# Kernel optimization log

Hardware: AMD Instinct MI355X
Metric: run time of the kernel (lower is better)

Reference implementation:

```python
import jax, jax.numpy as jnp
import numpy as np

N = 100000      # nodes
E = 1600000     # edges
IN, H, OUT = 128, 128, 64
P_DROP = 0.5


def _glorot_linear(key, out_d, in_d):
    # PyG Linear default init (kaiming-uniform-ish); exact init is irrelevant for the baseline
    bound = 1.0 / np.sqrt(in_d)
    return jax.random.uniform(key, (out_d, in_d), jnp.float32, -bound, bound)


def setup_inputs() -> dict:
    key = jax.random.key(0)
    ks = jax.random.split(key, 8)
    x = jax.random.normal(ks[0], (N, IN), jnp.float32)
    edge_index = jax.random.randint(ks[1], (2, E), 0, N, dtype=jnp.int64)
    W1l = _glorot_linear(ks[2], H, IN)
    b1 = jnp.zeros((H,), jnp.float32)
    W1r = _glorot_linear(ks[3], H, IN)
    W2l = _glorot_linear(ks[4], OUT, H)
    b2 = jnp.zeros((OUT,), jnp.float32)
    W2r = _glorot_linear(ks[5], OUT, H)
    return dict(x=x, edge_index=edge_index, W1l=W1l, b1=b1, W1r=W1r,
                W2l=W2l, b2=b2, W2r=W2r)


def _sage_conv(x, src, dst, Wl, bl, Wr):
    # PyG SAGEConv (aggr='mean'): out = lin_l(mean_{j in N(i)} x_j) + lin_r(x_i)
    msg = x[src]                                             # [E, d] gather
    agg = jax.ops.segment_sum(msg, dst, num_segments=N)      # [N, d] scatter-add
    cnt = jax.ops.segment_sum(jnp.ones((src.shape[0], 1), x.dtype), dst,
                              num_segments=N)                # [N, 1] in-degree
    mean = agg / jnp.maximum(cnt, 1.0)                       # isolated nodes -> 0
    return mean @ Wl.T + bl + x @ Wr.T


def reference(x, edge_index, W1l, b1, W1r, W2l, b2, W2r):
    src, dst = edge_index[0], edge_index[1]
    h = _sage_conv(x, src, dst, W1l, b1, W1r)
    h = jax.nn.relu(h)
    # F.dropout(p=0.5) made deterministic with a fixed key
    keep = jax.random.bernoulli(jax.random.key(42), 1.0 - P_DROP, h.shape)
    h = jnp.where(keep, h / (1.0 - P_DROP), 0.0)
    return _sage_conv(h, src, dst, W2l, b2, W2r)
```

## Files before the change

### kernel.cpp

```cpp
#include <hip/hip_runtime.h>
#include <hip/hip_bf16.h>

#define N_NODES 100000
#define NE      1600000

#define BINSH 7
#define NBIN  782
#define BCAP  3072
#define SEPB  16384
#define NBLK  ((NE + SEPB - 1) / SEPB)
#define NMASKW 200000

typedef __attribute__((ext_vector_type(8))) short bfrag;
typedef __attribute__((ext_vector_type(4))) float ffrag;

#define BFLO(u) __uint_as_float((u) << 16)
#define BFHI(u) __uint_as_float((u) & 0xffff0000u)

__device__ __forceinline__ unsigned tf_rotl(unsigned x, int d) {
    return (x << d) | (x >> (32 - d));
}

__device__ __forceinline__ unsigned tf_word(unsigned f) {
    const unsigned ks0 = 0u;
    const unsigned ks1 = 42u;
    const unsigned ks2 = 0x1BD11BDAu ^ 0u ^ 42u;
    unsigned x0 = 0u + ks0;
    unsigned x1 = f + ks1;
#define TF_RND(r) { x0 += x1; x1 = tf_rotl(x1, r); x1 ^= x0; }
    TF_RND(13) TF_RND(15) TF_RND(26) TF_RND(6)
    x0 += ks1; x1 += ks2 + 1u;
    TF_RND(17) TF_RND(29) TF_RND(16) TF_RND(24)
    x0 += ks2; x1 += ks0 + 2u;
    TF_RND(13) TF_RND(15) TF_RND(26) TF_RND(6)
    x0 += ks0; x1 += ks1 + 3u;
    TF_RND(17) TF_RND(29) TF_RND(16) TF_RND(24)
    x0 += ks1; x1 += ks2 + 4u;
    TF_RND(13) TF_RND(15) TF_RND(26) TF_RND(6)
    x0 += ks2; x1 += ks0 + 5u;
#undef TF_RND
    return x0 ^ x1;
}

__device__ __forceinline__ unsigned short bf_bits(float v) {
    __hip_bfloat16 b = __float2bfloat16(v);
    return *(unsigned short*)&b;
}

__global__ __launch_bounds__(256) void k_pre(
    const float4* __restrict__ x4, ushort4* __restrict__ xb4,
    const float* __restrict__ W1l, const float* __restrict__ W1r,
    const float* __restrict__ W2l, const float* __restrict__ W2r,
    __hip_bfloat16* __restrict__ wb,
    const int* __restrict__ ei, int* __restrict__ flag,
    int* __restrict__ bincur, unsigned long long* __restrict__ km) {
    const int tid0 = blockIdx.x * 256 + threadIdx.x;
    const int stride = gridDim.x * 256;

    for (int i = tid0; i < N_NODES * 128 / 4; i += stride) {
        float4 v = x4[i];
        ushort4 o;
        o.x = bf_bits(v.x); o.y = bf_bits(v.y);
        o.z = bf_bits(v.z); o.w = bf_bits(v.w);
        xb4[i] = o;
    }
    for (int i = tid0; i < 49152; i += stride) {
        float v;
        if (i < 16384)      v = W1l[i];
        else if (i < 32768) v = W1r[i - 16384];
        else if (i < 40960) v = W2l[i - 32768];
        else                v = W2r[i - 40960];
        wb[i] = __float2bfloat16(v);
    }
    if (blockIdx.x == 0) {
        __shared__ int nz;
        if (threadIdx.x == 0) nz = 0;
        __syncthreads();
        for (int i = threadIdx.x; i < 1024; i += 256) {
            if (ei[2 * i + 1] != 0) atomicAdd(&nz, 1);
            bincur[i] = 0;
        }
        __syncthreads();
        if (threadIdx.x == 0) *flag = (nz == 0) ? 1 : 0;
    }
    const int lane = threadIdx.x & 63;
    const int gw = tid0 >> 6;
    const int nw = stride >> 6;
    for (int widx = gw; widx < NMASKW; widx += nw) {
        unsigned wv = tf_word((unsigned)widx * 64u + (unsigned)lane);
        unsigned long long keep = __ballot(!(wv & 0x80000000u));
        if (lane == 0) km[widx] = keep;
    }
}

__global__ __launch_bounds__(1024) void k_binscatter(const int* __restrict__ ei,
        const int* __restrict__ flag, int* __restrict__ bincur,
        int* __restrict__ pairs) {
    __shared__ int h[NBIN];
    __shared__ int lbase[NBIN];
    for (int i = threadIdx.x; i < NBIN; i += 1024) h[i] = 0;
    __syncthreads();
    const int is64 = *flag;
    const int e0 = blockIdx.x * SEPB + threadIdx.x;
    int d[16], s[16];
#pragma unroll
    for (int k = 0; k < 16; ++k) {
        int e = e0 + k * 1024;
        if (e < NE) {
            d[k] = is64 ? ei[2 * (NE + e)] : ei[NE + e];
            s[k] = is64 ? ei[2 * e]        : ei[e];
            atomicAdd(&h[d[k] >> BINSH], 1);
        } else {
            d[k] = -1; s[k] = 0;
        }
    }
    __syncthreads();
    for (int i = threadIdx.x; i < NBIN; i += 1024) {
        int c = h[i];
        lbase[i] = c ? atomicAdd(&bincur[i], c) : 0;
        h[i] = 0;
    }
    __syncthreads();
#pragma unroll
    for (int k = 0; k < 16; ++k) {
        if (d[k] >= 0) {
            int b = d[k] >> BINSH;
            int r = atomicAdd(&h[b], 1);
            pairs[(size_t)b * BCAP + lbase[b] + r] =
                ((d[k] & 127) << 17) | s[k];
        }
    }
}

__global__ __launch_bounds__(1024) void k_aggcsr(
        const __hip_bfloat16* __restrict__ feat,
        const int* __restrict__ pairs, const int* __restrict__ bincnt,
        int* __restrict__ ptr, int* __restrict__ adj,
        __hip_bfloat16* __restrict__ mean) {
    __shared__ int ladj[BCAP];
    __shared__ int cnt[128];
    __shared__ int sc[128];
    __shared__ int woff[128];
    __shared__ int red[16];
    __shared__ int base_s;
    const int b = blockIdx.x;
    const int t = threadIdx.x;

    int s = 0;
    for (int i = t; i < b; i += 1024) s += bincnt[i];
#pragma unroll
    for (int off = 32; off > 0; off >>= 1) s += __shfl_down(s, off);
    if ((t & 63) == 0) red[t >> 6] = s;
    if (t < 128) cnt[t] = 0;
    __syncthreads();
    if (t == 0) {
        int tot = 0;
#pragma unroll
        for (int i = 0; i < 16; ++i) tot += red[i];
        base_s = tot;
    }
    __syncthreads();
    const int base = base_s;
    const int nb = bincnt[b];
    const int* pb = pairs + (size_t)b * BCAP;

    for (int i = t; i < nb; i += 1024)
        atomicAdd(&cnt[(pb[i] >> 17) & 127], 1);
    __syncthreads();
    if (t < 128) sc[t] = cnt[t];
    __syncthreads();
    for (int o = 1; o < 128; o <<= 1) {
        int u = 0;
        if (t < 128 && t >= o) u = sc[t - o];
        __syncthreads();
        if (t < 128) sc[t] += u;
        __syncthreads();
    }
    if (t < 128) {
        int ex = sc[t] - cnt[t];
        int node = b * 128 + t;
        if (node <= N_NODES) ptr[node] = base + ex;
        woff[t] = ex;
    }
    __syncthreads();
    for (int i = t; i < nb; i += 1024) {
        int pk = pb[i];
        int r = atomicAdd(&woff[(pk >> 17) & 127], 1);
        int src = pk & 0x1FFFF;
        ladj[r] = src;
        adj[base + r] = src;
    }
    __syncthreads();

    const int w = t >> 6;
    const int l = t & 63;
    const int half = l >> 5;
    const size_t coff = (size_t)(l & 31) * 4;
    for (int i = 0; i < 8; ++i) {
        const int local = w * 8 + i;
        const int node = b * 128 + local;
        if (node >= N_NODES) continue;
        const int p1 = sc[local];
        const int p0 = p1 - cnt[local];
        float c0 = 0.f, c1 = 0.f, c2 = 0.f, c3 = 0.f;
        float d0 = 0.f, d1 = 0.f, d2 = 0.f, d3 = 0.f;
        int p = p0;
        for (; p + 15 < p1; p += 16) {
            int sx[8];
#pragma unroll
            for (int k = 0; k < 8; ++k) sx[k] = ladj[p + 2 * k + half];
#pragma unroll
            for (int k = 0; k < 8; ++k) {
                uint2 u = *(const uint2*)(feat + (size_t)sx[k] * 128 + coff);
                if (k & 1) { d0 += BFLO(u.x); d1 += BFHI(u.x); d2 += BFLO(u.y); d3 += BFHI(u.y); }
                else       { c0 += BFLO(u.x); c1 += BFHI(u.x); c2 += BFLO(u.y); c3 += BFHI(u.y); }
            }
        }
        for (; p + 7 < p1; p += 8) {
            int sx[4];
#pragma unroll
            for (int k = 0; k < 4; ++k) sx[k] = ladj[p + 2 * k + half];
#pragma unroll
            for (int k = 0; k < 4; ++k) {
                uint2 u = *(const uint2*)(feat + (size_t)sx[k] * 128 + coff);
                if (k & 1) { d0 += BFLO(u.x); d1 += BFHI(u.x); d2 += BFLO(u.y); d3 += BFHI(u.y); }
                else       { c0 += BFLO(u.x); c1 += BFHI(u.x); c2 += BFLO(u.y); c3 += BFHI(u.y); }
            }
        }
        for (; p + 1 < p1; p += 2) {
            int sx = ladj[p + half];
            uint2 u = *(const uint2*)(feat + (size_t)sx * 128 + coff);
            c0 += BFLO(u.x); c1 += BFHI(u.x); c2 += BFLO(u.y); c3 += BFHI(u.y);
        }
        if (p < p1 && half == 0) {
            int sx = ladj[p];
            uint2 u = *(const uint2*)(feat + (size_t)sx * 128 + coff);
            c0 += BFLO(u.x); c1 += BFHI(u.x); c2 += BFLO(u.y); c3 += BFHI(u.y);
        }
        c0 += d0; c1 += d1; c2 += d2; c3 += d3;
        c0 += __shfl_xor(c0, 32);
        c1 += __shfl_xor(c1, 32);
        c2 += __shfl_xor(c2, 32);
        c3 += __shfl_xor(c3, 32);
        if (half == 0) {
            const float inv = 1.0f / (float)max(p1 - p0, 1);
            uint2 o;
            o.x = ((unsigned)bf_bits(c1 * inv) << 16) | (unsigned)bf_bits(c0 * inv);
            o.y = ((unsigned)bf_bits(c3 * inv) << 16) | (unsigned)bf_bits(c2 * inv);
            *(uint2*)(mean + (size_t)node * 128 + coff) = o;
        }
    }
}

__global__ __launch_bounds__(256) void k_lin1f(
    const __hip_bfloat16* __restrict__ Am, const __hip_bfloat16* __restrict__ Ax,
    const __hip_bfloat16* __restrict__ W1l, const __hip_bfloat16* __restrict__ W1r,
    const float* __restrict__ b1,
    const __hip_bfloat16* __restrict__ W2l, const __hip_bfloat16* __restrict__ W2r,
    const float* __restrict__ b2,
    const unsigned long long* __restrict__ kmask,
    __hip_bfloat16* __restrict__ y2, __hip_bfloat16* __restrict__ zb) {
    __shared__ __align__(16) __hip_bfloat16 hs[64][136];
    const int tid = threadIdx.x;
    const int w  = tid >> 6;
    const int l  = tid & 63;
    const int lr = l & 15;
    const int lk = l >> 4;
    const int j0 = w * 32;
    const int j2 = w * 16 + lr;
    const int n0 = blockIdx.x * 64;

    bfrag B1[2][2][4];
#pragma unroll
    for (int jt = 0; jt < 2; ++jt) {
        const int jrow = j0 + jt * 16 + lr;
#pragma unroll
        for (int ks = 0; ks < 4; ++ks) {
            B1[jt][0][ks] = *(const bfrag*)(W1l + jrow * 128 + ks * 32 + lk * 8);
            B1[jt][1][ks] = *(const bfrag*)(W1r + jrow * 128 + ks * 32 + lk * 8);
        }
    }
    bfrag Bl2[4], Br2[4];
#pragma unroll
    for (int ks = 0; ks < 4; ++ks) {
        Bl2[ks] = *(const bfrag*)(W2l + j2 * 128 + ks * 32 + lk * 8);
        Br2[ks] = *(const bfrag*)(W2r + j2 * 128 + ks * 32 + lk * 8);
    }
    const float bj0 = b1[j0 + lr];
    const float bj1 = b1[j0 + 16 + lr];
    const float bj2 = b2[j2];

    for (int t = 0; t < 4; ++t) {
        const int rbase = n0 + t * 16;
        int arow = rbase + lr;
        if (arow > N_NODES - 1) arow = N_NODES - 1;
        ffrag acc0 = {0.f, 0.f, 0.f, 0.f};
        ffrag acc1 = {0.f, 0.f, 0.f, 0.f};
#pragma unroll
        for (int ks = 0; ks < 4; ++ks) {
            bfrag am = *(const bfrag*)(Am + (size_t)arow * 128 + ks * 32 + lk * 8);
            bfrag ax = *(const bfrag*)(Ax + (size_t)arow * 128 + ks * 32 + lk * 8);
            acc0 = __builtin_amdgcn_mfma_f32_16x16x32_bf16(am, B1[0][0][ks], acc0, 0, 0, 0);
            acc1 = __builtin_amdgcn_mfma_f32_16x16x32_bf16(am, B1[1][0][ks], acc1, 0, 0, 0);
            acc0 = __builtin_amdgcn_mfma_f32_16x16x32_bf16(ax, B1[0][1][ks], acc0, 0, 0, 0);
            acc1 = __builtin_amdgcn_mfma_f32_16x16x32_bf16(ax, B1[1][1][ks], acc1, 0, 0, 0);
        }
#pragma unroll
        for (int r = 0; r < 4; ++r) {
            const int n = rbase + lk * 4 + r;
            const int lrow = t * 16 + lk * 4 + r;
            const int nm = (n < N_NODES) ? n : (N_NODES - 1);
            const unsigned long long km = kmask[nm * 2 + (j0 >> 6)];
            float v0 = fmaxf(acc0[r] + bj0, 0.f);
            v0 = ((km >> ((j0 + lr) & 63)) & 1ull) ? (v0 + v0) : 0.f;
            hs[lrow][j0 + lr] = __float2bfloat16(v0);
            float v1 = fmaxf(acc1[r] + bj1, 0.f);
            v1 = ((km >> ((j0 + 16 + lr) & 63)) & 1ull) ? (v1 + v1) : 0.f;
            hs[lrow][j0 + 16 + lr] = __float2bfloat16(v1);
        }
    }
    __syncthreads();

    for (int t = 0; t < 4; ++t) {
        ffrag accY = {0.f, 0.f, 0.f, 0.f};
        ffrag accZ = {0.f, 0.f, 0.f, 0.f};
#pragma unroll
        for (int ks = 0; ks < 4; ++ks) {
            bfrag ah = *(const bfrag*)&hs[t * 16 + lr][ks * 32 + lk * 8];
            accY = __builtin_amdgcn_mfma_f32_16x16x32_bf16(ah, Bl2[ks], accY, 0, 0, 0);
            accZ = __builtin_amdgcn_mfma_f32_16x16x32_bf16(ah, Br2[ks], accZ, 0, 0, 0);
        }
#pragma unroll
        for (int r = 0; r < 4; ++r) {
            const int n = n0 + t * 16 + lk * 4 + r;
            if (n < N_NODES) {
                y2[(size_t)n * 64 + j2] = __float2bfloat16(accY[r]);
                zb[(size_t)n * 64 + j2] = __float2bfloat16(accZ[r] + bj2);
            }
        }
    }
}

__global__ void k_agg2f(const __hip_bfloat16* __restrict__ feat,
                        const int* __restrict__ ptr, const int* __restrict__ adj,
                        const __hip_bfloat16* __restrict__ zb,
                        float* __restrict__ out) {
    const int node = (blockIdx.x * blockDim.x + threadIdx.x) >> 5;
    const int sl = threadIdx.x & 31;
    if (node >= N_NODES) return;
    const int p0 = ptr[node], p1 = ptr[node + 1];
    const int sub = sl >> 4;
    const size_t coff = (size_t)(sl & 15) * 4;
    float c0 = 0.f, c1 = 0.f, c2 = 0.f, c3 = 0.f;
    float d0 = 0.f, d1 = 0.f, d2 = 0.f, d3 = 0.f;
    int p = p0;
    for (; p + 15 < p1; p += 16) {
        int s[8];
#pragma unroll
        for (int k = 0; k < 8; ++k) s[k] = adj[p + 2 * k + sub];
#pragma unroll
        for (int k = 0; k < 8; ++k) {
            uint2 u = *(const uint2*)(feat + (size_t)s[k] * 64 + coff);
            if (k & 1) { d0 += BFLO(u.x); d1 += BFHI(u.x); d2 += BFLO(u.y); d3 += BFHI(u.y); }
            else       { c0 += BFLO(u.x); c1 += BFHI(u.x); c2 += BFLO(u.y); c3 += BFHI(u.y); }
        }
    }
    for (; p + 7 < p1; p += 8) {
        int s[4];
#pragma unroll
        for (int k = 0; k < 4; ++k) s[k] = adj[p + 2 * k + sub];
#pragma unroll
        for (int k = 0; k < 4; ++k) {
            uint2 u = *(const uint2*)(feat + (size_t)s[k] * 64 + coff);
            if (k & 1) { d0 += BFLO(u.x); d1 += BFHI(u.x); d2 += BFLO(u.y); d3 += BFHI(u.y); }
            else       { c0 += BFLO(u.x); c1 += BFHI(u.x); c2 += BFLO(u.y); c3 += BFHI(u.y); }
        }
    }
    for (; p + 1 < p1; p += 2) {
        int s = adj[p + sub];
        uint2 u = *(const uint2*)(feat + (size_t)s * 64 + coff);
        c0 += BFLO(u.x); c1 += BFHI(u.x); c2 += BFLO(u.y); c3 += BFHI(u.y);
    }
    if (p < p1 && sub == 0) {
        int s = adj[p];
        uint2 u = *(const uint2*)(feat + (size_t)s * 64 + coff);
        c0 += BFLO(u.x); c1 += BFHI(u.x); c2 += BFLO(u.y); c3 += BFHI(u.y);
    }
    c0 += d0; c1 += d1; c2 += d2; c3 += d3;
    c0 += __shfl_xor(c0, 16);
    c1 += __shfl_xor(c1, 16);
    c2 += __shfl_xor(c2, 16);
    c3 += __shfl_xor(c3, 16);
    if (sub == 0) {
        const float inv = 1.0f / (float)max(p1 - p0, 1);
        uint2 zu = *(const uint2*)(zb + (size_t)node * 64 + coff);
        float4 o;
        o.x = BFLO(zu.x) + c0 * inv;
        o.y = BFHI(zu.x) + c1 * inv;
        o.z = BFLO(zu.y) + c2 * inv;
        o.w = BFHI(zu.y) + c3 * inv;
        *(float4*)(out + (size_t)node * 64 + coff) = o;
    }
}

extern "C" void kernel_launch(void* const* d_in, const int* in_sizes, int n_in,
                              void* d_out, int out_size, void* d_ws, size_t ws_size,
                              hipStream_t stream) {
    const float* x   = (const float*)d_in[0];
    const int*   ei  = (const int*)d_in[1];
    const float* W1l = (const float*)d_in[2];
    const float* b1  = (const float*)d_in[3];
    const float* W1r = (const float*)d_in[4];
    const float* W2l = (const float*)d_in[5];
    const float* b2  = (const float*)d_in[6];
    const float* W2r = (const float*)d_in[7];
    float* out = (float*)d_out;

    char* w = (char*)d_ws;
    int* flag   = (int*)w;
    int* bincur = flag + 64;
    int* ptr    = bincur + 1024;
    int* adj    = ptr + (N_NODES + 1);
    size_t koff = (((size_t)(64 + 1024 + N_NODES + 1 + NE)) * 4 + 255)
                  & ~(size_t)255;
    unsigned long long* kmask = (unsigned long long*)(w + koff);
    size_t foff = (koff + (size_t)NMASKW * 8 + 255) & ~(size_t)255;
    __hip_bfloat16* wb    = (__hip_bfloat16*)(w + foff);
    __hip_bfloat16* w1lb  = wb;
    __hip_bfloat16* w1rb  = wb + 16384;
    __hip_bfloat16* w2lb  = wb + 32768;
    __hip_bfloat16* w2rb  = wb + 40960;
    __hip_bfloat16* xb    = wb + 49152;
    __hip_bfloat16* meanb = xb + (size_t)N_NODES * 128;
    char* pregion = (char*)(meanb + (size_t)N_NODES * 128);
    int* pairs = (int*)pregion;
    __hip_bfloat16* y2b = (__hip_bfloat16*)pregion;
    __hip_bfloat16* zbb = y2b + (size_t)N_NODES * 64;

    k_pre<<<2048, 256, 0, stream>>>((const float4*)x, (ushort4*)xb,
                                    W1l, W1r, W2l, W2r, wb,
                                    ei, flag, bincur, kmask);

    k_binscatter<<<NBLK, 1024, 0, stream>>>(ei, flag, bincur, pairs);

    k_aggcsr<<<NBIN, 1024, 0, stream>>>(xb, pairs, bincur, ptr, adj, meanb);

    const int nb  = (N_NODES + 63) / 64;
    const int ab2 = (N_NODES + 7) / 8;

    k_lin1f<<<nb, 256, 0, stream>>>(meanb, xb, w1lb, w1rb, b1,
                                    w2lb, w2rb, b2, kmask, y2b, zbb);
    k_agg2f<<<ab2, 256, 0, stream>>>(y2b, ptr, adj, zbb, out);
}
```

Baseline: 231.1 us.

## Merge preprocessing with bin scatter and split CSR aggregation blocks in half

Merges the conversion/mask kernel and the edge bin-scatter kernel into one launch. Blocks are partitioned by index: the first ones scatter edges, the rest convert features and weights and build the dropout mask, so the two jobs run side by side. Each block now detects int64 edge indices locally, and bincur is zeroed by a memset. The CSR aggregation grid is doubled so each bin is handled by two blocks, each owning 64 nodes. This raises parallelism, but both blocks redo the prefix sums and bin scans, and per-node occupancy drops.

```diff
diff --git a/kernel.cpp b/kernel.cpp
--- a/kernel.cpp
+++ b/kernel.cpp
@@ -8,7 +8,8 @@
 #define NBIN  782
 #define BCAP  3072
 #define SEPB  16384
-#define NBLK  ((NE + SEPB - 1) / SEPB)
+#define SC_BLKS ((NE + SEPB - 1) / SEPB)
+#define PRE_BLKS 512
 #define NMASKW 200000
 
 typedef __attribute__((ext_vector_type(8))) short bfrag;
@@ -47,87 +48,79 @@
     return *(unsigned short*)&b;
 }
 
-__global__ __launch_bounds__(256) void k_pre(
+__global__ __launch_bounds__(1024) void k_prescatter(
+    const int* __restrict__ ei, int* __restrict__ bincur, int* __restrict__ pairs,
     const float4* __restrict__ x4, ushort4* __restrict__ xb4,
     const float* __restrict__ W1l, const float* __restrict__ W1r,
     const float* __restrict__ W2l, const float* __restrict__ W2r,
-    __hip_bfloat16* __restrict__ wb,
-    const int* __restrict__ ei, int* __restrict__ flag,
-    int* __restrict__ bincur, unsigned long long* __restrict__ km) {
-    const int tid0 = blockIdx.x * 256 + threadIdx.x;
-    const int stride = gridDim.x * 256;
-
-    for (int i = tid0; i < N_NODES * 128 / 4; i += stride) {
-        float4 v = x4[i];
-        ushort4 o;
-        o.x = bf_bits(v.x); o.y = bf_bits(v.y);
-        o.z = bf_bits(v.z); o.w = bf_bits(v.w);
-        xb4[i] = o;
-    }
-    for (int i = tid0; i < 49152; i += stride) {
-        float v;
-        if (i < 16384)      v = W1l[i];
-        else if (i < 32768) v = W1r[i - 16384];
-        else if (i < 40960) v = W2l[i - 32768];
-        else                v = W2r[i - 40960];
-        wb[i] = __float2bfloat16(v);
-    }
-    if (blockIdx.x == 0) {
+    __hip_bfloat16* __restrict__ wb, unsigned long long* __restrict__ km) {
+    const int t = threadIdx.x;
+
+    if (blockIdx.x < SC_BLKS) {
         __shared__ int nz;
-        if (threadIdx.x == 0) nz = 0;
-        __syncthreads();
-        for (int i = threadIdx.x; i < 1024; i += 256) {
-            if (ei[2 * i + 1] != 0) atomicAdd(&nz, 1);
-            bincur[i] = 0;
-        }
-        __syncthreads();
-        if (threadIdx.x == 0) *flag = (nz == 0) ? 1 : 0;
-    }
-    const int lane = threadIdx.x & 63;
-    const int gw = tid0 >> 6;
-    const int nw = stride >> 6;
-    for (int widx = gw; widx < NMASKW; widx += nw) {
-        unsigned wv = tf_word((unsigned)widx * 64u + (unsigned)lane);
-        unsigned long long keep = __ballot(!(wv & 0x80000000u));
-        if (lane == 0) km[widx] = keep;
-    }
-}
-
-__global__ __launch_bounds__(1024) void k_binscatter(const int* __restrict__ ei,
-        const int* __restrict__ flag, int* __restrict__ bincur,
-        int* __restrict__ pairs) {
-    __shared__ int h[NBIN];
-    __shared__ int lbase[NBIN];
-    for (int i = threadIdx.x; i < NBIN; i += 1024) h[i] = 0;
-    __syncthreads();
-    const int is64 = *flag;
-    const int e0 = blockIdx.x * SEPB + threadIdx.x;
-    int d[16], s[16];
-#pragma unroll
-    for (int k = 0; k < 16; ++k) {
-        int e = e0 + k * 1024;
-        if (e < NE) {
-            d[k] = is64 ? ei[2 * (NE + e)] : ei[NE + e];
-            s[k] = is64 ? ei[2 * e]        : ei[e];
-            atomicAdd(&h[d[k] >> BINSH], 1);
-        } else {
-            d[k] = -1; s[k] = 0;
-        }
-    }
-    __syncthreads();
-    for (int i = threadIdx.x; i < NBIN; i += 1024) {
-        int c = h[i];
-        lbase[i] = c ? atomicAdd(&bincur[i], c) : 0;
-        h[i] = 0;
-    }
-    __syncthreads();
-#pragma unroll
-    for (int k = 0; k < 16; ++k) {
-        if (d[k] >= 0) {
-            int b = d[k] >> BINSH;
-            int r = atomicAdd(&h[b], 1);
-            pairs[(size_t)b * BCAP + lbase[b] + r] =
-                ((d[k] & 127) << 17) | s[k];
+        __shared__ int h[NBIN];
+        __shared__ int lbase[NBIN];
+        if (t == 0) nz = 0;
+        for (int i = t; i < NBIN; i += 1024) h[i] = 0;
+        __syncthreads();
+        if (t < 1024 && ei[2 * t + 1] != 0) atomicAdd(&nz, 1);
+        __syncthreads();
+        const int is64 = (nz == 0) ? 1 : 0;
+
+        const int e0 = blockIdx.x * SEPB + t;
+        int d[16], s[16];
+#pragma unroll
+        for (int k = 0; k < 16; ++k) {
+            int e = e0 + k * 1024;
+            if (e < NE) {
+                d[k] = is64 ? ei[2 * (NE + e)] : ei[NE + e];
+                s[k] = is64 ? ei[2 * e]        : ei[e];
+                atomicAdd(&h[d[k] >> BINSH], 1);
+            } else {
+                d[k] = -1; s[k] = 0;
+            }
+        }
+        __syncthreads();
+        for (int i = t; i < NBIN; i += 1024) {
+            int c = h[i];
+            lbase[i] = c ? atomicAdd(&bincur[i], c) : 0;
+            h[i] = 0;
+        }
+        __syncthreads();
+#pragma unroll
+        for (int k = 0; k < 16; ++k) {
+            if (d[k] >= 0) {
+                int b = d[k] >> BINSH;
+                int r = atomicAdd(&h[b], 1);
+                pairs[(size_t)b * BCAP + lbase[b] + r] =
+                    ((d[k] & 127) << 17) | s[k];
+            }
+        }
+    } else {
+        const int tid0 = (blockIdx.x - SC_BLKS) * 1024 + t;
+        const int stride = (PRE_BLKS - SC_BLKS) * 1024;
+        for (int i = tid0; i < N_NODES * 128 / 4; i += stride) {
+            float4 v = x4[i];
+            ushort4 o;
+            o.x = bf_bits(v.x); o.y = bf_bits(v.y);
+            o.z = bf_bits(v.z); o.w = bf_bits(v.w);
+            xb4[i] = o;
+        }
+        for (int i = tid0; i < 49152; i += stride) {
+            float v;
+            if (i < 16384)      v = W1l[i];
+            else if (i < 32768) v = W1r[i - 16384];
+            else if (i < 40960) v = W2l[i - 32768];
+            else                v = W2r[i - 40960];
+            wb[i] = __float2bfloat16(v);
+        }
+        const int lane = t & 63;
+        const int gw = tid0 >> 6;
+        const int nw = stride >> 6;
+        for (int widx = gw; widx < NMASKW; widx += nw) {
+            unsigned wv = tf_word((unsigned)widx * 64u + (unsigned)lane);
+            unsigned long long keep = __ballot(!(wv & 0x80000000u));
+            if (lane == 0) km[widx] = keep;
         }
     }
 }
@@ -143,7 +136,8 @@
     __shared__ int woff[128];
     __shared__ int red[16];
     __shared__ int base_s;
-    const int b = blockIdx.x;
+    const int b = blockIdx.x >> 1;
+    const int hb = blockIdx.x & 1;
     const int t = threadIdx.x;
 
     int s = 0;
@@ -179,16 +173,19 @@
     if (t < 128) {
         int ex = sc[t] - cnt[t];
         int node = b * 128 + t;
-        if (node <= N_NODES) ptr[node] = base + ex;
+        if (hb == ((t >> 6) & 1) && node <= N_NODES) ptr[node] = base + ex;
         woff[t] = ex;
     }
     __syncthreads();
     for (int i = t; i < nb; i += 1024) {
         int pk = pb[i];
-        int r = atomicAdd(&woff[(pk >> 17) & 127], 1);
-        int src = pk & 0x1FFFF;
-        ladj[r] = src;
-        adj[base + r] = src;
+        int dl = (pk >> 17) & 127;
+        if ((dl >> 6) == hb) {
+            int r = atomicAdd(&woff[dl], 1);
+            int src = pk & 0x1FFFF;
+            ladj[r] = src;
+            adj[base + r] = src;
+        }
     }
     __syncthreads();
 
@@ -196,8 +193,8 @@
     const int l = t & 63;
     const int half = l >> 5;
     const size_t coff = (size_t)(l & 31) * 4;
-    for (int i = 0; i < 8; ++i) {
-        const int local = w * 8 + i;
+    for (int i = 0; i < 4; ++i) {
+        const int local = hb * 64 + w * 4 + i;
         const int node = b * 128 + local;
         if (node >= N_NODES) continue;
         const int p1 = sc[local];
@@ -417,8 +414,7 @@
     float* out = (float*)d_out;
 
     char* w = (char*)d_ws;
-    int* flag   = (int*)w;
-    int* bincur = flag + 64;
+    int* bincur = (int*)w + 64;
     int* ptr    = bincur + 1024;
     int* adj    = ptr + (N_NODES + 1);
     size_t koff = (((size_t)(64 + 1024 + N_NODES + 1 + NE)) * 4 + 255)
@@ -437,13 +433,13 @@
     __hip_bfloat16* y2b = (__hip_bfloat16*)pregion;
     __hip_bfloat16* zbb = y2b + (size_t)N_NODES * 64;
 
-    k_pre<<<2048, 256, 0, stream>>>((const float4*)x, (ushort4*)xb,
-                                    W1l, W1r, W2l, W2r, wb,
-                                    ei, flag, bincur, kmask);
-
-    k_binscatter<<<NBLK, 1024, 0, stream>>>(ei, flag, bincur, pairs);
-
-    k_aggcsr<<<NBIN, 1024, 0, stream>>>(xb, pairs, bincur, ptr, adj, meanb);
+    hipMemsetAsync(bincur, 0, 1024 * sizeof(int), stream);
+
+    k_prescatter<<<PRE_BLKS, 1024, 0, stream>>>(ei, bincur, pairs,
+                                                (const float4*)x, (ushort4*)xb,
+                                                W1l, W1r, W2l, W2r, wb, kmask);
+
+    k_aggcsr<<<NBIN * 2, 1024, 0, stream>>>(xb, pairs, bincur, ptr, adj, meanb);
 
     const int nb  = (N_NODES + 63) / 64;
     const int ab2 = (N_NODES + 7) / 8;
```

Result: faster. 223.3 us (-3.4%).
